# Kernel optimization log

Measured on AMD Instinct MI355X. Metric: run time of the kernel, lower is better.

Reference implementation:

```python
import jax, jax.numpy as jnp
import numpy as np

B, N, F_IN, F_OUT = 16, 1024, 256, 256
ALPHA = 0.2  # leakyrelu negative slope
NEG_BIG = -9e15


def setup_inputs() -> dict:
    key = jax.random.key(0)
    k1, k2, k3, k4 = jax.random.split(key, 4)
    h = jax.random.normal(k1, (B, N, F_IN), dtype=jnp.float32)
    adj = jax.random.randint(k2, (B, N, N), 0, 2, dtype=jnp.int32)
    # xavier_uniform with gain=1.414
    def xavier(k, shape, gain=1.414):
        fan_in, fan_out = shape[0], shape[1]
        bound = gain * np.sqrt(6.0 / (fan_in + fan_out))
        return jax.random.uniform(k, shape, dtype=jnp.float32, minval=-bound, maxval=bound)
    W = xavier(k3, (F_IN, F_OUT))
    a = xavier(k4, (2 * F_OUT, 1))
    return {"h": h, "adj": adj, "W": W, "a": a}


def reference(h, adj, W, a):
    Wh = jnp.matmul(h, W)  # [B, N, F_OUT]
    # a^T [Wh_i ; Wh_j] = a1^T Wh_i + a2^T Wh_j -- avoids O(N^2 * 2F) concat tensor
    a1 = a[:F_OUT, 0]  # [F_OUT]
    a2 = a[F_OUT:, 0]  # [F_OUT]
    e_i = jnp.einsum('bnf,f->bn', Wh, a1)  # score contribution of source node i
    e_j = jnp.einsum('bnf,f->bn', Wh, a2)  # score contribution of target node j
    e = e_i[:, :, None] + e_j[:, None, :]  # [B, N, N]
    e = jnp.where(e > 0, e, ALPHA * e)  # leaky relu
    e = jnp.where(adj > 0, e, NEG_BIG)
    attention = jax.nn.softmax(e, axis=2)
    h_prime = jnp.matmul(attention, Wh)  # [B, N, F_OUT]
    return jax.nn.elu(h_prime)  # concat=True
```

## Files before the change

kernel.cpp:

```cpp
#include <hip/hip_runtime.h>
#include <hip/hip_bf16.h>

#define B_ 16
#define N_ 1024
#define F_ 256
#define ALPHA 0.2f
#define NEG_BIG -9.0e15f
#define LOG2E 1.4426950408889634f

typedef float f4 __attribute__((ext_vector_type(4)));
typedef float f32x4 __attribute__((ext_vector_type(4)));
typedef short s16x8 __attribute__((ext_vector_type(8)));
typedef short s16x4 __attribute__((ext_vector_type(4)));

__device__ inline short f2bs(float x) {
    __hip_bfloat16 h = __float2bfloat16(x);
    return __builtin_bit_cast(short, h);
}

__global__ __launch_bounds__(256) void k_wa(const float* __restrict__ W,
                                            const float* __restrict__ a,
                                            float* __restrict__ wa) {
    const int t = threadIdx.x, lane = t & 63, w = t >> 6;
    const int row = blockIdx.x * 4 + w;
    const f4 wv = *(const f4*)(W + (size_t)row * F_ + lane * 4);
    const f4 a1 = *(const f4*)(a + lane * 4);
    const f4 a2 = *(const f4*)(a + F_ + lane * 4);
    float s1 = wv[0]*a1[0] + wv[1]*a1[1] + wv[2]*a1[2] + wv[3]*a1[3];
    float s2 = wv[0]*a2[0] + wv[1]*a2[1] + wv[2]*a2[2] + wv[3]*a2[3];
#pragma unroll
    for (int off = 32; off > 0; off >>= 1) {
        s1 += __shfl_xor(s1, off);
        s2 += __shfl_xor(s2, off);
    }
    if (lane == 0) { wa[row] = s1; wa[256 + row] = s2; }
}

__global__ __launch_bounds__(256) void k_gemm(const float* __restrict__ h,
                                              const float* __restrict__ W,
                                              unsigned short* __restrict__ WhT) {
    __shared__ unsigned short sA[64 * 64];
    __shared__ unsigned short sB[64 * 64];
    const int t = threadIdx.x, l = t & 63, w = t >> 6;
    const int m0 = blockIdx.x * 64, f0 = blockIdx.y * 64;
    const int jg = l >> 4, li = l & 15;
    f32x4 acc[4] = {};

    for (int kt = 0; kt < 4; ++kt) {
        const int k0 = kt * 64;
        if (kt) __syncthreads();
#pragma unroll
        for (int r = 0; r < 2; ++r) {
            const int c = t * 2 + r;
            const int m = c >> 3, kc = c & 7;
            const f4 lo = *(const f4*)(h + (size_t)(m0 + m) * F_ + k0 + kc * 8);
            const f4 hi = *(const f4*)(h + (size_t)(m0 + m) * F_ + k0 + kc * 8 + 4);
            s16x8 v;
            v[0]=f2bs(lo[0]); v[1]=f2bs(lo[1]); v[2]=f2bs(lo[2]); v[3]=f2bs(lo[3]);
            v[4]=f2bs(hi[0]); v[5]=f2bs(hi[1]); v[6]=f2bs(hi[2]); v[7]=f2bs(hi[3]);
            *(s16x8*)((char*)sA + m * 128 + ((kc ^ (m & 7)) << 4)) = v;
        }
        {
            const int kr = (t >> 4) * 4, fc = (t & 15) * 4;
            f4 r0 = *(const f4*)(W + (size_t)(k0 + kr + 0) * F_ + f0 + fc);
            f4 r1 = *(const f4*)(W + (size_t)(k0 + kr + 1) * F_ + f0 + fc);
            f4 r2 = *(const f4*)(W + (size_t)(k0 + kr + 2) * F_ + f0 + fc);
            f4 r3 = *(const f4*)(W + (size_t)(k0 + kr + 3) * F_ + f0 + fc);
#pragma unroll
            for (int ff = 0; ff < 4; ++ff) {
                const int f = fc + ff;
                s16x4 v;
                v[0]=f2bs(r0[ff]); v[1]=f2bs(r1[ff]); v[2]=f2bs(r2[ff]); v[3]=f2bs(r3[ff]);
                *(s16x4*)((char*)sB + f * 128 + (((kr >> 3) ^ (f & 7)) << 4) + (kr & 7) * 2) = v;
            }
        }
        __syncthreads();
        const int mloc = w * 16 + li;
#pragma unroll
        for (int ks = 0; ks < 2; ++ks) {
            const int kchunk = ks * 4 + jg;
            const s16x8 av = *(const s16x8*)((const char*)sA + mloc * 128 + ((kchunk ^ (mloc & 7)) << 4));
#pragma unroll
            for (int ft = 0; ft < 4; ++ft) {
                const int f = ft * 16 + li;
                const s16x8 bv = *(const s16x8*)((const char*)sB + f * 128 + ((kchunk ^ (f & 7)) << 4));
                acc[ft] = __builtin_amdgcn_mfma_f32_16x16x32_bf16(av, bv, acc[ft], 0, 0, 0);
            }
        }
    }
    const int bb = m0 >> 10;
    const int mb = (m0 & 1023) + w * 16 + jg * 4;
#pragma unroll
    for (int ft = 0; ft < 4; ++ft) {
        const int fg = f0 + ft * 16 + li;
        s16x4 v;
        v[0]=f2bs(acc[ft][0]); v[1]=f2bs(acc[ft][1]);
        v[2]=f2bs(acc[ft][2]); v[3]=f2bs(acc[ft][3]);
        *(s16x4*)(WhT + ((size_t)(bb * 256 + fg)) * 1024 + mb) = v;
    }
}

__global__ __launch_bounds__(256) void k_e2(const float* __restrict__ h,
                                            const float* __restrict__ wa,
                                            float* __restrict__ ei,
                                            float* __restrict__ ej) {
    const int lane = threadIdx.x & 63;
    const int row = blockIdx.x * 4 + (threadIdx.x >> 6);
    const f4 hv = *(const f4*)(h + (size_t)row * F_ + lane * 4);
    const f4 w1 = *(const f4*)(wa + lane * 4);
    const f4 w2 = *(const f4*)(wa + 256 + lane * 4);
    float s1 = hv[0]*w1[0] + hv[1]*w1[1] + hv[2]*w1[2] + hv[3]*w1[3];
    float s2 = hv[0]*w2[0] + hv[1]*w2[1] + hv[2]*w2[2] + hv[3]*w2[3];
#pragma unroll
    for (int off = 32; off > 0; off >>= 1) {
        s1 += __shfl_xor(s1, off);
        s2 += __shfl_xor(s2, off);
    }
    if (lane == 0) { ei[row] = s1 * LOG2E; ej[row] = s2 * LOG2E; }
}

__global__ __launch_bounds__(256) void k_attn(const unsigned short* __restrict__ WhT,
                                              const float* __restrict__ ei_g,
                                              const float* __restrict__ ej_g,
                                              const int* __restrict__ adj,
                                              float* __restrict__ out) {
    const int id = blockIdx.x;
    const int xcd = id & 7, slot = id >> 3;
    const int b = xcd * 2 + (slot >> 5);
    const int i0 = (slot & 31) * 32;

    __shared__ unsigned short sT[2 * 16384];

    const int t = threadIdx.x, l = t & 63, w = t >> 6;
    const int ih = w >> 1, fbase = (w & 1) * 128;
    const int li = l & 15, jg = l >> 4;
    const int irow = i0 + ih * 16 + li;

    const unsigned short* whb = WhT + (size_t)b * F_ * N_;
    const int* adjrow = adj + ((size_t)b * N_ + irow) * N_;
    const float* ejb = ej_g + b * N_;
    const float eival = ei_g[b * N_ + irow];

    const unsigned short* gsrc[8];
    int ldst[8];
#pragma unroll
    for (int r = 0; r < 8; ++r) {
        const int c0 = (w * 8 + r) * 64;
        const int c = c0 + l;
        const int f_o = c >> 3;
        const int jc_s = (c & 7) ^ (f_o & 7);
        gsrc[r] = whb + (size_t)f_o * N_ + jc_s * 8;
        ldst[r] = c0 * 16;
    }
    auto stage = [&](int j0, int buf) {
#pragma unroll
        for (int r = 0; r < 8; ++r) {
            __builtin_amdgcn_global_load_lds(
                (const __attribute__((address_space(1))) unsigned int*)(gsrc[r] + j0),
                (__attribute__((address_space(3))) unsigned int*)((char*)sT + buf * 32768 + ldst[r]),
                16, 0, 0);
        }
    };

    float m = NEG_BIG, ll = 0.f;
    f32x4 acc[8] = {};

    stage(0, 0);
    int4 adjc[4];
    f4 ejc[4];
#pragma unroll
    for (int q = 0; q < 4; ++q) {
        adjc[q] = *(const int4*)(adjrow + (q >> 1) * 32 + jg * 8 + (q & 1) * 4);
        ejc[q] = *(const f4*)(ejb + (q >> 1) * 32 + jg * 8 + (q & 1) * 4);
    }
    __syncthreads();

    for (int s = 0; s < 16; ++s) {
        const int cur = s & 1;
        int4 adjn[4];
        f4 ejn[4];
        if (s < 15) {
            stage((s + 1) * 64, cur ^ 1);
            const int j0n = (s + 1) * 64;
#pragma unroll
            for (int q = 0; q < 4; ++q) {
                adjn[q] = *(const int4*)(adjrow + j0n + (q >> 1) * 32 + jg * 8 + (q & 1) * 4);
                ejn[q] = *(const f4*)(ejb + j0n + (q >> 1) * 32 + jg * 8 + (q & 1) * 4);
            }
        }
#pragma unroll
        for (int sub = 0; sub < 2; ++sub) {
            const f4 ej0 = ejc[sub * 2], ej1 = ejc[sub * 2 + 1];
            const int4 a0 = adjc[sub * 2], a1 = adjc[sub * 2 + 1];
            float p[8];
            float tm = NEG_BIG;
#pragma unroll
            for (int e = 0; e < 8; ++e) {
                const float ejv = (e < 4) ? ej0[e] : ej1[e - 4];
                float sc = eival + ejv;
                sc = fmaxf(sc, ALPHA * sc);
                const int ad = (e < 4) ? ((const int*)&a0)[e] : ((const int*)&a1)[e - 4];
                sc = ad > 0 ? sc : NEG_BIG;
                p[e] = sc;
                tm = fmaxf(tm, sc);
            }
            tm = fmaxf(tm, __shfl_xor(tm, 16));
            tm = fmaxf(tm, __shfl_xor(tm, 32));
            if (__any(tm > m + 11.5f)) {
                const float mn = fmaxf(m, tm);
                const float fac = __builtin_amdgcn_exp2f(m - mn);
                m = mn;
                ll *= fac;
                float fr[4];
#pragma unroll
                for (int q = 0; q < 4; ++q) fr[q] = __shfl(fac, jg * 4 + q);
#pragma unroll
                for (int ft = 0; ft < 8; ++ft)
#pragma unroll
                    for (int q = 0; q < 4; ++q) acc[ft][q] *= fr[q];
            }
            float sum = 0.f;
            s16x8 afrag;
#pragma unroll
            for (int e = 0; e < 8; ++e) {
                const float pe = __builtin_amdgcn_exp2f(p[e] - m);
                afrag[e] = f2bs(pe);
                sum += pe;
            }
            sum += __shfl_xor(sum, 16);
            sum += __shfl_xor(sum, 32);
            ll += sum;
#pragma unroll
            for (int ft = 0; ft < 8; ++ft) {
                const int f = fbase + ft * 16 + li;
                const int jcr = sub * 4 + jg;
                const s16x8 bv = *(const s16x8*)((const char*)sT + cur * 32768 + f * 128 + ((jcr ^ (f & 7)) << 4));
                acc[ft] = __builtin_amdgcn_mfma_f32_16x16x32_bf16(afrag, bv, acc[ft], 0, 0, 0);
            }
        }
        if (s < 15) {
#pragma unroll
            for (int q = 0; q < 4; ++q) { adjc[q] = adjn[q]; ejc[q] = ejn[q]; }
        }
        __syncthreads();
    }

    const float il = 1.f / ll;
    float inv[4];
#pragma unroll
    for (int q = 0; q < 4; ++q) inv[q] = __shfl(il, jg * 4 + q);
#pragma unroll
    for (int ft = 0; ft < 8; ++ft) {
#pragma unroll
        for (int q = 0; q < 4; ++q) {
            float v = acc[ft][q] * inv[q];
            v = v > 0.f ? v : __builtin_amdgcn_exp2f(v * LOG2E) - 1.f;
            out[((size_t)b * N_ + i0 + ih * 16 + jg * 4 + q) * F_ + fbase + ft * 16 + li] = v;
        }
    }
}

extern "C" void kernel_launch(void* const* d_in, const int* in_sizes, int n_in,
                              void* d_out, int out_size, void* d_ws, size_t ws_size,
                              hipStream_t stream) {
    const float* h = (const float*)d_in[0];
    const int* adj = (const int*)d_in[1];
    const float* W = (const float*)d_in[2];
    const float* a = (const float*)d_in[3];
    float* out = (float*)d_out;

    unsigned short* WhT = (unsigned short*)d_ws;
    float* wa = (float*)(WhT + (size_t)B_ * N_ * F_);
    float* ei = wa + 512;
    float* ej = ei + (size_t)B_ * N_;

    k_wa<<<64, 256, 0, stream>>>(W, a, wa);
    k_gemm<<<dim3(256, 4), 256, 0, stream>>>(h, W, WhT);
    k_e2<<<(B_ * N_) / 4, 256, 0, stream>>>(h, wa, ei, ej);
    k_attn<<<512, 256, 0, stream>>>(WhT, ei, ej, adj, out);
}
```

Before: 160.9 us.

## Drop LDS staging: pre-transpose W to bf16, read MFMA operands directly from global

Adds a small kernel that transposes W into bf16 once, so the projection GEMM can load h and W fragments straight from global memory into registers with no shared-memory tiles or barriers. Each GEMM block now covers 32 rows by all 256 features. The attention kernel likewise drops its double-buffered global-to-LDS staging of WhT and the per-step __syncthreads, loading B fragments directly from global and relying on L2 reuse across waves. The aim is to remove LDS and barrier overhead and raise occupancy, with launch_bounds now asking for 4 blocks per CU. The cost is less explicit latency hiding and more redundant global or L2 traffic.

```diff
diff --git a/kernel.cpp b/kernel.cpp
--- a/kernel.cpp
+++ b/kernel.cpp
@@ -36,63 +36,60 @@
     if (lane == 0) { wa[row] = s1; wa[256 + row] = s2; }
 }
 
-__global__ __launch_bounds__(256) void k_gemm(const float* __restrict__ h,
-                                              const float* __restrict__ W,
-                                              unsigned short* __restrict__ WhT) {
-    __shared__ unsigned short sA[64 * 64];
-    __shared__ unsigned short sB[64 * 64];
+__global__ __launch_bounds__(256) void k_wt(const float* __restrict__ W,
+                                            unsigned short* __restrict__ WTb) {
+    __shared__ float tile[64][65];
+    const int t = threadIdx.x;
+    const int k0 = (blockIdx.x >> 2) * 64, f0 = (blockIdx.x & 3) * 64;
+#pragma unroll
+    for (int rep = 0; rep < 4; ++rep) {
+        const int idx = rep * 256 + t;
+        const int kr = idx >> 4, fc = (idx & 15) * 4;
+        const f4 v = *(const f4*)(W + (size_t)(k0 + kr) * F_ + f0 + fc);
+        tile[kr][fc] = v[0]; tile[kr][fc + 1] = v[1];
+        tile[kr][fc + 2] = v[2]; tile[kr][fc + 3] = v[3];
+    }
+    __syncthreads();
+#pragma unroll
+    for (int rep = 0; rep < 4; ++rep) {
+        const int idx = rep * 256 + t;
+        const int fr = idx >> 4, kc = (idx & 15) * 4;
+        s16x4 v;
+        v[0] = f2bs(tile[kc][fr]);     v[1] = f2bs(tile[kc + 1][fr]);
+        v[2] = f2bs(tile[kc + 2][fr]); v[3] = f2bs(tile[kc + 3][fr]);
+        *(s16x4*)(WTb + (size_t)(f0 + fr) * F_ + k0 + kc) = v;
+    }
+}
+
+__global__ __launch_bounds__(256, 4) void k_gemm(const float* __restrict__ h,
+                                                 const unsigned short* __restrict__ WTb,
+                                                 unsigned short* __restrict__ WhT) {
     const int t = threadIdx.x, l = t & 63, w = t >> 6;
-    const int m0 = blockIdx.x * 64, f0 = blockIdx.y * 64;
-    const int jg = l >> 4, li = l & 15;
-    f32x4 acc[4] = {};
-
-    for (int kt = 0; kt < 4; ++kt) {
-        const int k0 = kt * 64;
-        if (kt) __syncthreads();
-#pragma unroll
-        for (int r = 0; r < 2; ++r) {
-            const int c = t * 2 + r;
-            const int m = c >> 3, kc = c & 7;
-            const f4 lo = *(const f4*)(h + (size_t)(m0 + m) * F_ + k0 + kc * 8);
-            const f4 hi = *(const f4*)(h + (size_t)(m0 + m) * F_ + k0 + kc * 8 + 4);
-            s16x8 v;
-            v[0]=f2bs(lo[0]); v[1]=f2bs(lo[1]); v[2]=f2bs(lo[2]); v[3]=f2bs(lo[3]);
-            v[4]=f2bs(hi[0]); v[5]=f2bs(hi[1]); v[6]=f2bs(hi[2]); v[7]=f2bs(hi[3]);
-            *(s16x8*)((char*)sA + m * 128 + ((kc ^ (m & 7)) << 4)) = v;
-        }
-        {
-            const int kr = (t >> 4) * 4, fc = (t & 15) * 4;
-            f4 r0 = *(const f4*)(W + (size_t)(k0 + kr + 0) * F_ + f0 + fc);
-            f4 r1 = *(const f4*)(W + (size_t)(k0 + kr + 1) * F_ + f0 + fc);
-            f4 r2 = *(const f4*)(W + (size_t)(k0 + kr + 2) * F_ + f0 + fc);
-            f4 r3 = *(const f4*)(W + (size_t)(k0 + kr + 3) * F_ + f0 + fc);
-#pragma unroll
-            for (int ff = 0; ff < 4; ++ff) {
-                const int f = fc + ff;
-                s16x4 v;
-                v[0]=f2bs(r0[ff]); v[1]=f2bs(r1[ff]); v[2]=f2bs(r2[ff]); v[3]=f2bs(r3[ff]);
-                *(s16x4*)((char*)sB + f * 128 + (((kr >> 3) ^ (f & 7)) << 4) + (kr & 7) * 2) = v;
-            }
-        }
-        __syncthreads();
-        const int mloc = w * 16 + li;
-#pragma unroll
-        for (int ks = 0; ks < 2; ++ks) {
-            const int kchunk = ks * 4 + jg;
-            const s16x8 av = *(const s16x8*)((const char*)sA + mloc * 128 + ((kchunk ^ (mloc & 7)) << 4));
-#pragma unroll
-            for (int ft = 0; ft < 4; ++ft) {
-                const int f = ft * 16 + li;
-                const s16x8 bv = *(const s16x8*)((const char*)sB + f * 128 + ((kchunk ^ (f & 7)) << 4));
-                acc[ft] = __builtin_amdgcn_mfma_f32_16x16x32_bf16(av, bv, acc[ft], 0, 0, 0);
-            }
+    const int ih = w >> 1, fh = w & 1;
+    const int m0 = blockIdx.x * 32;
+    const int li = l & 15, jg = l >> 4;
+    const int mrow = m0 + ih * 16 + li;
+    const float* hrow = h + (size_t)mrow * F_ + jg * 8;
+    const unsigned short* bbase = WTb + (size_t)(fh * 128 + li) * F_ + jg * 8;
+    f32x4 acc[8] = {};
+#pragma unroll
+    for (int kk = 0; kk < 8; ++kk) {
+        const f4 lo = *(const f4*)(hrow + kk * 32);
+        const f4 hi = *(const f4*)(hrow + kk * 32 + 4);
+        s16x8 av;
+        av[0]=f2bs(lo[0]); av[1]=f2bs(lo[1]); av[2]=f2bs(lo[2]); av[3]=f2bs(lo[3]);
+        av[4]=f2bs(hi[0]); av[5]=f2bs(hi[1]); av[6]=f2bs(hi[2]); av[7]=f2bs(hi[3]);
+#pragma unroll
+        for (int ft = 0; ft < 8; ++ft) {
+            const s16x8 bv = *(const s16x8*)(bbase + (size_t)ft * 16 * F_ + kk * 32);
+            acc[ft] = __builtin_amdgcn_mfma_f32_16x16x32_bf16(av, bv, acc[ft], 0, 0, 0);
         }
     }
     const int bb = m0 >> 10;
-    const int mb = (m0 & 1023) + w * 16 + jg * 4;
-#pragma unroll
-    for (int ft = 0; ft < 4; ++ft) {
-        const int fg = f0 + ft * 16 + li;
+    const int mb = (m0 & 1023) + ih * 16 + jg * 4;
+#pragma unroll
+    for (int ft = 0; ft < 8; ++ft) {
+        const int fg = fh * 128 + ft * 16 + li;
         s16x4 v;
         v[0]=f2bs(acc[ft][0]); v[1]=f2bs(acc[ft][1]);
         v[2]=f2bs(acc[ft][2]); v[3]=f2bs(acc[ft][3]);
@@ -119,18 +116,16 @@
     if (lane == 0) { ei[row] = s1 * LOG2E; ej[row] = s2 * LOG2E; }
 }
 
-__global__ __launch_bounds__(256) void k_attn(const unsigned short* __restrict__ WhT,
-                                              const float* __restrict__ ei_g,
-                                              const float* __restrict__ ej_g,
-                                              const int* __restrict__ adj,
-                                              float* __restrict__ out) {
+__global__ __launch_bounds__(256, 4) void k_attn(const unsigned short* __restrict__ WhT,
+                                                 const float* __restrict__ ei_g,
+                                                 const float* __restrict__ ej_g,
+                                                 const int* __restrict__ adj,
+                                                 float* __restrict__ out) {
     const int id = blockIdx.x;
     const int xcd = id & 7, slot = id >> 3;
     const int b = xcd * 2 + (slot >> 5);
     const int i0 = (slot & 31) * 32;
 
-    __shared__ unsigned short sT[2 * 16384];
-
     const int t = threadIdx.x, l = t & 63, w = t >> 6;
     const int ih = w >> 1, fbase = (w & 1) * 128;
     const int li = l & 15, jg = l >> 4;
@@ -141,31 +136,14 @@
     const float* ejb = ej_g + b * N_;
     const float eival = ei_g[b * N_ + irow];
 
-    const unsigned short* gsrc[8];
-    int ldst[8];
-#pragma unroll
-    for (int r = 0; r < 8; ++r) {
-        const int c0 = (w * 8 + r) * 64;
-        const int c = c0 + l;
-        const int f_o = c >> 3;
-        const int jc_s = (c & 7) ^ (f_o & 7);
-        gsrc[r] = whb + (size_t)f_o * N_ + jc_s * 8;
-        ldst[r] = c0 * 16;
-    }
-    auto stage = [&](int j0, int buf) {
-#pragma unroll
-        for (int r = 0; r < 8; ++r) {
-            __builtin_amdgcn_global_load_lds(
-                (const __attribute__((address_space(1))) unsigned int*)(gsrc[r] + j0),
-                (__attribute__((address_space(3))) unsigned int*)((char*)sT + buf * 32768 + ldst[r]),
-                16, 0, 0);
-        }
-    };
+    const unsigned short* bptr[8];
+#pragma unroll
+    for (int ft = 0; ft < 8; ++ft)
+        bptr[ft] = whb + (size_t)(fbase + ft * 16 + li) * N_ + jg * 8;
 
     float m = NEG_BIG, ll = 0.f;
     f32x4 acc[8] = {};
 
-    stage(0, 0);
     int4 adjc[4];
     f4 ejc[4];
 #pragma unroll
@@ -173,14 +151,11 @@
         adjc[q] = *(const int4*)(adjrow + (q >> 1) * 32 + jg * 8 + (q & 1) * 4);
         ejc[q] = *(const f4*)(ejb + (q >> 1) * 32 + jg * 8 + (q & 1) * 4);
     }
-    __syncthreads();
 
     for (int s = 0; s < 16; ++s) {
-        const int cur = s & 1;
         int4 adjn[4];
         f4 ejn[4];
         if (s < 15) {
-            stage((s + 1) * 64, cur ^ 1);
             const int j0n = (s + 1) * 64;
 #pragma unroll
             for (int q = 0; q < 4; ++q) {
@@ -232,9 +207,7 @@
             ll += sum;
 #pragma unroll
             for (int ft = 0; ft < 8; ++ft) {
-                const int f = fbase + ft * 16 + li;
-                const int jcr = sub * 4 + jg;
-                const s16x8 bv = *(const s16x8*)((const char*)sT + cur * 32768 + f * 128 + ((jcr ^ (f & 7)) << 4));
+                const s16x8 bv = *(const s16x8*)(bptr[ft] + s * 64 + sub * 32);
                 acc[ft] = __builtin_amdgcn_mfma_f32_16x16x32_bf16(afrag, bv, acc[ft], 0, 0, 0);
             }
         }
@@ -242,7 +215,6 @@
 #pragma unroll
             for (int q = 0; q < 4; ++q) { adjc[q] = adjn[q]; ejc[q] = ejn[q]; }
         }
-        __syncthreads();
     }
 
     const float il = 1.f / ll;
@@ -273,9 +245,11 @@
     float* wa = (float*)(WhT + (size_t)B_ * N_ * F_);
     float* ei = wa + 512;
     float* ej = ei + (size_t)B_ * N_;
+    unsigned short* WTb = (unsigned short*)(ej + (size_t)B_ * N_);
 
     k_wa<<<64, 256, 0, stream>>>(W, a, wa);
-    k_gemm<<<dim3(256, 4), 256, 0, stream>>>(h, W, WhT);
+    k_wt<<<16, 256, 0, stream>>>(W, WTb);
+    k_gemm<<<512, 256, 0, stream>>>(h, WTb, WhT);
     k_e2<<<(B_ * N_) / 4, 256, 0, stream>>>(h, wa, ei, ej);
     k_attn<<<512, 256, 0, stream>>>(WhT, ei, ej, adj, out);
 }
```

Measured after the change: 210.9 us. 31.0% more time.
